# Optimization experiments

Measured on AMD Instinct MI355X. Metric: run time of the kernel, lower is better.

## Reference

```python
import jax, jax.numpy as jnp
import numpy as np
import math

B, S, D, H, KV, HD = 2, 2048, 2048, 32, 8, 64
N_REP = H // KV


def setup_inputs() -> dict:
    key = jax.random.key(0)
    ks = jax.random.split(key, 6)
    x = jax.random.normal(ks[0], (B, S, D), jnp.float32)
    # torch Linear weights, stored as [in, out] for x @ w
    wq = jax.random.normal(ks[1], (D, H * HD), jnp.float32) * 0.02
    wk = jax.random.normal(ks[2], (D, KV * HD), jnp.float32) * 0.02
    wv = jax.random.normal(ks[3], (D, KV * HD), jnp.float32) * 0.02
    wo = jax.random.normal(ks[4], (H * HD, D), jnp.float32) * 0.02
    # rotary angle table: theta[t, j] = t / 10000^(2j/head_dim)
    inv_freq = 1.0 / (10000.0 ** (jnp.arange(0, HD, 2, dtype=jnp.float32) / HD))
    freqs = jnp.arange(S, dtype=jnp.float32)[:, None] * inv_freq[None, :]  # [S, HD//2]
    mask = jnp.triu(jnp.full((S, S), -1e9, dtype=jnp.float32), k=1)
    return {"x": x, "wq": wq, "wk": wk, "wv": wv, "wo": wo,
            "freqs": freqs, "mask": mask, "start_pos": 0}


def _apply_rope(t, cos, sin):
    # t: [b, s, h, d]; pairs are adjacent (llama complex convention)
    b, s, h, d = t.shape
    t2 = t.reshape(b, s, h, d // 2, 2)
    tr, ti = t2[..., 0], t2[..., 1]
    c = cos[None, :, None, :]
    sn = sin[None, :, None, :]
    out_r = tr * c - ti * sn
    out_i = tr * sn + ti * c
    return jnp.stack([out_r, out_i], axis=-1).reshape(b, s, h, d)


def reference(x, wq, wk, wv, wo, freqs, mask, start_pos):
    bsz, seqlen, _ = x.shape
    cos, sin = jnp.cos(freqs), jnp.sin(freqs)
    xq = (x @ wq).reshape(bsz, seqlen, H, HD)
    xk = (x @ wk).reshape(bsz, seqlen, KV, HD)
    xv = (x @ wv).reshape(bsz, seqlen, KV, HD)
    xq = _apply_rope(xq, cos, sin)
    xk = _apply_rope(xk, cos, sin)
    # start_pos == 0 prefill: cache slice [:start_pos+seqlen] == fresh k/v
    keys = jnp.repeat(xk, N_REP, axis=2)    # [b, s, H, hd]
    values = jnp.repeat(xv, N_REP, axis=2)
    q = xq.transpose(0, 2, 1, 3)            # [b, H, s, hd]
    k = keys.transpose(0, 2, 1, 3)
    v = values.transpose(0, 2, 1, 3)
    scores = jnp.einsum('bhqd,bhkd->bhqk', q, k) / math.sqrt(HD)
    scores = scores + mask[None, None, :, :]
    probs = jax.nn.softmax(scores.astype(jnp.float32), axis=-1).astype(q.dtype)
    out = jnp.einsum('bhqk,bhkd->bhqd', probs, v)
    out = out.transpose(0, 2, 1, 3).reshape(bsz, seqlen, H * HD)
    return out @ wo
```

## Files before the change

kernel.cpp:

```cpp
#include <hip/hip_runtime.h>

typedef __attribute__((ext_vector_type(8))) __bf16 bf16x8;
typedef __attribute__((ext_vector_type(4)))  float f32x4;
typedef __attribute__((ext_vector_type(16))) float f32x16;

__device__ __forceinline__ unsigned short f2bfu(float x) {
  union { float f; unsigned u; } v; v.f = x;
  unsigned r = v.u + 0x7fffu + ((v.u >> 16) & 1u);
  return (unsigned short)(r >> 16);
}
__device__ __forceinline__ float bf2f(unsigned short u) {
  union { unsigned u; float f; } v; v.u = ((unsigned)u) << 16;
  return v.f;
}
__device__ __forceinline__ unsigned pkbf(float a, float b) {
  return (unsigned)f2bfu(a) | ((unsigned)f2bfu(b) << 16);
}
__device__ __forceinline__ unsigned pk2(float a, float b) {
  union { __bf16 h[2]; unsigned u; } t;
  t.h[0] = (__bf16)a; t.h[1] = (__bf16)b;
  return t.u;
}
__device__ __forceinline__ void gload16(const void* g, void* l) {
  __builtin_amdgcn_global_load_lds((const __attribute__((address_space(1))) unsigned*)g,
                                   (__attribute__((address_space(3))) unsigned*)l, 16, 0, 0);
}
__device__ __forceinline__ bf16x8 mk8(unsigned a, unsigned b, unsigned c, unsigned d) {
  union { unsigned u[4]; bf16x8 v; } t;
  t.u[0] = a; t.u[1] = b; t.u[2] = c; t.u[3] = d; return t.v;
}

__global__ void cvt_kernel(const float* __restrict__ s, short* __restrict__ d, int n) {
  int i = (blockIdx.x * 256 + threadIdx.x) * 4;
  if (i >= n) return;
  float4 v = *(const float4*)(s + i);
  short4 o;
  o.x = (short)f2bfu(v.x); o.y = (short)f2bfu(v.y);
  o.z = (short)f2bfu(v.z); o.w = (short)f2bfu(v.w);
  *(short4*)(d + i) = o;
}

__global__ void transcvt_kernel(const float* __restrict__ src, short* __restrict__ dst,
                                int R, int C) {
  __shared__ __align__(16) float tl[64][65];
  int c0 = blockIdx.x * 64, r0 = blockIdx.y * 64;
  int t = threadIdx.x;
  int tr = t >> 4, tc = (t & 15) * 4;
#pragma unroll
  for (int i = 0; i < 4; i++) {
    int r = i * 16 + tr;
    float4 v = *(const float4*)(src + (size_t)(r0 + r) * C + c0 + tc);
    tl[r][tc] = v.x; tl[r][tc + 1] = v.y; tl[r][tc + 2] = v.z; tl[r][tc + 3] = v.w;
  }
  __syncthreads();
#pragma unroll
  for (int i = 0; i < 4; i++) {
    int cr = i * 16 + tr;
    short4 o;
    o.x = (short)f2bfu(tl[tc][cr]);
    o.y = (short)f2bfu(tl[tc + 1][cr]);
    o.z = (short)f2bfu(tl[tc + 2][cr]);
    o.w = (short)f2bfu(tl[tc + 3][cr]);
    *(short4*)(dst + (size_t)(c0 + cr) * R + r0 + tc) = o;
  }
}

__global__ void sincos_kernel(const float* __restrict__ freqs, float* __restrict__ ct,
                              float* __restrict__ st) {
  int i = blockIdx.x * 256 + threadIdx.x;
  float f = freqs[i];
  ct[i] = cosf(f);
  st[i] = sinf(f);
}

template <int OUTF32>
__global__ __launch_bounds__(256) void gemm_bt(const short* __restrict__ A,
                                               const short* __restrict__ Bt,
                                               void* __restrict__ C, int M, int N, int K) {
  __shared__ __align__(16) short Al[128 * 32];
  __shared__ __align__(16) short Bl[128 * 32];
  const int t = threadIdx.x, lane = t & 63, w = t >> 6;
  const int m0 = blockIdx.x * 128, n0 = blockIdx.y * 128;
  const int wm = (w & 1) * 64, wn = (w >> 1) * 64;
  f32x4 acc[4][4];
#pragma unroll
  for (int i = 0; i < 4; i++)
#pragma unroll
    for (int j = 0; j < 4; j++)
#pragma unroll
      for (int r = 0; r < 4; r++) acc[i][j][r] = 0.f;

  const int sr = t >> 2;
  const int ss = t & 3;
  const int ldsbase = w * 512;

  for (int k0 = 0; k0 < K; k0 += 32) {
    __syncthreads();
#pragma unroll
    for (int p = 0; p < 2; p++) {
      int r = p * 64 + sr;
      int c = 8 * (ss ^ ((r >> 1) & 3));
      gload16(A + (size_t)(m0 + r) * K + k0 + c, &Al[p * 2048 + ldsbase]);
      gload16(Bt + (size_t)(n0 + r) * K + k0 + c, &Bl[p * 2048 + ldsbase]);
    }
    __syncthreads();
    bf16x8 af[4], bg[4];
#pragma unroll
    for (int i = 0; i < 4; i++) {
      int ra = wm + i * 16 + (lane & 15);
      int sa = (lane >> 4) ^ ((ra >> 1) & 3);
      af[i] = *(const bf16x8*)(&Al[ra * 32 + sa * 8]);
      int rb = wn + i * 16 + (lane & 15);
      int sb = (lane >> 4) ^ ((rb >> 1) & 3);
      bg[i] = *(const bf16x8*)(&Bl[rb * 32 + sb * 8]);
    }
#pragma unroll
    for (int i = 0; i < 4; i++)
#pragma unroll
      for (int j = 0; j < 4; j++)
        acc[i][j] = __builtin_amdgcn_mfma_f32_16x16x32_bf16(af[i], bg[j], acc[i][j], 0, 0, 0);
  }
  const int cr = (lane >> 4) * 4, cc = lane & 15;
#pragma unroll
  for (int i = 0; i < 4; i++)
#pragma unroll
    for (int j = 0; j < 4; j++)
#pragma unroll
      for (int r = 0; r < 4; r++) {
        size_t idx = (size_t)(m0 + wm + i * 16 + cr + r) * N + (n0 + wn + j * 16 + cc);
        if (OUTF32) ((float*)C)[idx] = acc[i][j][r];
        else        ((short*)C)[idx] = (short)f2bfu(acc[i][j][r]);
      }
}

__global__ void rope_kernel(short* __restrict__ qkv, const float* __restrict__ ct,
                            const float* __restrict__ st) {
  int idx = blockIdx.x * 256 + threadIdx.x;
  const int PQ = 4096 * 1024;
  int row, col, i;
  if (idx < PQ) {
    row = idx >> 10; int p = idx & 1023; int h = p >> 5; i = p & 31;
    col = h * 64 + 2 * i;
  } else {
    int k = idx - PQ; row = k >> 8; int p = k & 255; int kvh = p >> 5; i = p & 31;
    col = 2048 + kvh * 64 + 2 * i;
  }
  int s = row & 2047;
  unsigned* ptr = (unsigned*)(qkv + (size_t)row * 3072 + col);
  unsigned v = *ptr;
  float tr = bf2f((unsigned short)(v & 0xffff));
  float ti = bf2f((unsigned short)(v >> 16));
  float c = ct[(s << 5) + i], sn = st[(s << 5) + i];
  *ptr = pkbf(tr * c - ti * sn, tr * sn + ti * c);
}

__global__ void transv_kernel(const short* __restrict__ qkv, short* __restrict__ vt) {
  __shared__ __align__(16) short tl[64][72];
  int st0 = blockIdx.x * 64;
  int bkv = blockIdx.y; int b = bkv >> 3, kv = bkv & 7;
  int t = threadIdx.x;
  int rr = t >> 3, c8 = (t & 7) * 8;
#pragma unroll
  for (int i = 0; i < 2; i++) {
    int sl = i * 32 + rr;
    bf16x8 v = *(const bf16x8*)(qkv + (size_t)(b * 2048 + st0 + sl) * 3072 + 2560 + kv * 64 + c8);
    union { bf16x8 v; short s[8]; } u; u.v = v;
#pragma unroll
    for (int j = 0; j < 8; j++) tl[sl][c8 + j] = u.s[j];
  }
  __syncthreads();
#pragma unroll
  for (int i = 0; i < 2; i++) {
    int dl = i * 32 + rr;
    union { bf16x8 v; short s[8]; } o;
#pragma unroll
    for (int j = 0; j < 8; j++) o.s[j] = tl[c8 + j][dl];
    *(bf16x8*)(vt + ((size_t)(bkv * 64 + dl)) * 2048 + st0 + c8) = o.v;
  }
}

__global__ __launch_bounds__(256) void attn_kernel(const short* __restrict__ qkv,
                                                   const short* __restrict__ vt,
                                                   short* __restrict__ attn) {
  const int S = 2048, NC = 3072;
  __shared__ __align__(16) short sh[2][2][64 * 64];

  const int y = blockIdx.y;
  const int qi = (y < 8) ? y : (23 - y);
  const int qb = qi * 128;
  const int h = blockIdx.x, b = blockIdx.z;
  const int kvh = h >> 2;
  const int t = threadIdx.x, lane = t & 63, w = t >> 6;
  const int q0 = qb + w * 32;
  const int qc = lane & 31, hi = lane >> 5;
  const int qg = q0 + qc;

  bf16x8 bq[4];
  {
    const short* qp = qkv + (size_t)(b * S + qg) * NC + h * 64 + hi * 8;
    const float SC = 0.18033688011112042f;
#pragma unroll
    for (int kk = 0; kk < 4; kk++) {
      union { bf16x8 v; unsigned short s[8]; } u, o;
      u.v = *(const bf16x8*)(qp + kk * 16);
#pragma unroll
      for (int j = 0; j < 8; j++) o.s[j] = f2bfu(bf2f(u.s[j]) * SC);
      bq[kk] = o.v;
    }
  }

  f32x16 ot0, ot1;
#pragma unroll
  for (int r = 0; r < 16; r++) { ot0[r] = 0.f; ot1[r] = 0.f; }
  float m = -1e30f, l = 0.f;

  const int r8 = lane >> 3, sl8 = lane & 7;
  const int scol0 = 8 * (sl8 ^ ((r8 + w) & 7));
  const int scol1 = 8 * (sl8 ^ ((r8 + 4 + w) & 7));
  const short* kptr = qkv + (size_t)(b * S + w * 8 + r8) * NC + 2048 + kvh * 64;
  const short* vptr = vt + (size_t)((b * 8 + kvh) * 64 + w * 8 + r8) * S;

  const int nt = (qb >> 6) + 2;

#define STAGE(tt, bb)                                                                   \
  do {                                                                                  \
    gload16(kptr + (size_t)((tt) * 64) * NC + scol0,        &sh[bb][0][(w * 8) * 64]);  \
    gload16(kptr + (size_t)((tt) * 64 + 32) * NC + scol1,   &sh[bb][0][(32 + w * 8) * 64]); \
    gload16(vptr + (size_t)(tt) * 64 + scol0,               &sh[bb][1][(w * 8) * 64]);  \
    gload16(vptr + (size_t)32 * S + (tt) * 64 + scol1,      &sh[bb][1][(32 + w * 8) * 64]); \
  } while (0)

  STAGE(0, 0);
  __syncthreads();

  for (int tt = 0; tt < nt; ++tt) {
    const int cur = tt & 1;
    if (tt + 1 < nt) STAGE(tt + 1, cur ^ 1);
    const int s0 = tt * 64;
    const short* kb = &sh[cur][0][0];
    const short* vb = &sh[cur][1][0];

    f32x16 cs0, cs1;
#pragma unroll
    for (int r = 0; r < 16; r++) { cs0[r] = 0.f; cs1[r] = 0.f; }
    const int kr0 = lane & 31, kr1 = kr0 + 32;
    const int sw0 = (kr0 + (kr0 >> 3)) & 7, sw1 = (kr1 + (kr1 >> 3)) & 7;
#pragma unroll
    for (int kk = 0; kk < 4; kk++) {
      bf16x8 a0 = *(const bf16x8*)(kb + kr0 * 64 + ((2 * kk + hi) ^ sw0) * 8);
      cs0 = __builtin_amdgcn_mfma_f32_32x32x16_bf16(a0, bq[kk], cs0, 0, 0, 0);
      bf16x8 a1 = *(const bf16x8*)(kb + kr1 * 64 + ((2 * kk + hi) ^ sw1) * 8);
      cs1 = __builtin_amdgcn_mfma_f32_32x32x16_bf16(a1, bq[kk], cs1, 0, 0, 0);
    }

    if (s0 + 63 > q0) {
      const int qrel = qg - s0;
#pragma unroll
      for (int r = 0; r < 16; r++) {
        const int k0 = (r & 3) + 8 * (r >> 2) + 4 * hi;
        if (k0 > qrel)      cs0[r] = -1e30f;
        if (k0 + 32 > qrel) cs1[r] = -1e30f;
      }
    }

    float mx = fmaxf(cs0[0], cs1[0]);
#pragma unroll
    for (int r = 1; r < 16; r++) mx = fmaxf(mx, fmaxf(cs0[r], cs1[r]));
    mx = fmaxf(mx, __shfl_xor(mx, 32, 64));
    if (!__all(mx - m <= 8.f)) {
      const float mn = fmaxf(m, mx);
      const float rf = exp2f(m - mn);
      m = mn;
      l *= rf;
#pragma unroll
      for (int r = 0; r < 16; r++) { ot0[r] *= rf; ot1[r] *= rf; }
    }
    float ls = 0.f;
#pragma unroll
    for (int r = 0; r < 16; r++) { cs0[r] = exp2f(cs0[r] - m); ls += cs0[r]; }
#pragma unroll
    for (int r = 0; r < 16; r++) { cs1[r] = exp2f(cs1[r] - m); ls += cs1[r]; }
    l += ls;

    unsigned x0[8], y0[8], x1[8], y1[8];
#pragma unroll
    for (int j = 0; j < 8; j++) x0[j] = pk2(cs0[2 * j], cs0[2 * j + 1]);
#pragma unroll
    for (int j = 0; j < 8; j++) y0[j] = (unsigned)__shfl_xor((int)x0[j], 32, 64);
#pragma unroll
    for (int j = 0; j < 8; j++) x1[j] = pk2(cs1[2 * j], cs1[2 * j + 1]);
#pragma unroll
    for (int j = 0; j < 8; j++) y1[j] = (unsigned)__shfl_xor((int)x1[j], 32, 64);
    bf16x8 pb0 = hi ? mk8(y0[2], y0[3], x0[2], x0[3]) : mk8(x0[0], x0[1], y0[0], y0[1]);
    bf16x8 pb1 = hi ? mk8(y0[6], y0[7], x0[6], x0[7]) : mk8(x0[4], x0[5], y0[4], y0[5]);
    bf16x8 pb2 = hi ? mk8(y1[2], y1[3], x1[2], x1[3]) : mk8(x1[0], x1[1], y1[0], y1[1]);
    bf16x8 pb3 = hi ? mk8(y1[6], y1[7], x1[6], x1[7]) : mk8(x1[4], x1[5], y1[4], y1[5]);

    const int dl = lane & 31;
    {
      const int d = dl;
      const int swd = (d + (d >> 3)) & 7;
      bf16x8 v0 = *(const bf16x8*)(vb + d * 64 + ((0 + hi) ^ swd) * 8);
      bf16x8 v1 = *(const bf16x8*)(vb + d * 64 + ((2 + hi) ^ swd) * 8);
      bf16x8 v2 = *(const bf16x8*)(vb + d * 64 + ((4 + hi) ^ swd) * 8);
      bf16x8 v3 = *(const bf16x8*)(vb + d * 64 + ((6 + hi) ^ swd) * 8);
      ot0 = __builtin_amdgcn_mfma_f32_32x32x16_bf16(v0, pb0, ot0, 0, 0, 0);
      ot0 = __builtin_amdgcn_mfma_f32_32x32x16_bf16(v1, pb1, ot0, 0, 0, 0);
      ot0 = __builtin_amdgcn_mfma_f32_32x32x16_bf16(v2, pb2, ot0, 0, 0, 0);
      ot0 = __builtin_amdgcn_mfma_f32_32x32x16_bf16(v3, pb3, ot0, 0, 0, 0);
    }
    {
      const int d = 32 + dl;
      const int swd = (d + (d >> 3)) & 7;
      bf16x8 v0 = *(const bf16x8*)(vb + d * 64 + ((0 + hi) ^ swd) * 8);
      bf16x8 v1 = *(const bf16x8*)(vb + d * 64 + ((2 + hi) ^ swd) * 8);
      bf16x8 v2 = *(const bf16x8*)(vb + d * 64 + ((4 + hi) ^ swd) * 8);
      bf16x8 v3 = *(const bf16x8*)(vb + d * 64 + ((6 + hi) ^ swd) * 8);
      ot1 = __builtin_amdgcn_mfma_f32_32x32x16_bf16(v0, pb0, ot1, 0, 0, 0);
      ot1 = __builtin_amdgcn_mfma_f32_32x32x16_bf16(v1, pb1, ot1, 0, 0, 0);
      ot1 = __builtin_amdgcn_mfma_f32_32x32x16_bf16(v2, pb2, ot1, 0, 0, 0);
      ot1 = __builtin_amdgcn_mfma_f32_32x32x16_bf16(v3, pb3, ot1, 0, 0, 0);
    }
    __syncthreads();
  }
#undef STAGE

  short (*ol)[32 * 72] = (short (*)[32 * 72]) & sh[0][0][0];
  float lt = l + __shfl_xor(l, 32, 64);
  float inv = 1.0f / lt;
#pragma unroll
  for (int dh = 0; dh < 2; dh++) {
#pragma unroll
    for (int j = 0; j < 8; j++) {
      int d = ((2 * j) & 3) + 8 * ((2 * j) >> 2) + 4 * hi + 32 * dh;
      float a = (dh ? ot1[2 * j] : ot0[2 * j]) * inv;
      float bb = (dh ? ot1[2 * j + 1] : ot0[2 * j + 1]) * inv;
      *(unsigned*)(&ol[w][qc * 72 + d]) = pkbf(a, bb);
    }
  }
  __syncthreads();
  const int qr = lane >> 1, part = lane & 1;
  short* og = attn + (size_t)(b * S + q0 + qr) * 2048 + h * 64 + part * 32;
  const short* ip = &ol[w][qr * 72 + part * 32];
#pragma unroll
  for (int i2 = 0; i2 < 4; i2++) *(bf16x8*)(og + i2 * 8) = *(const bf16x8*)(ip + i2 * 8);
}

extern "C" void kernel_launch(void* const* d_in, const int* in_sizes, int n_in,
                              void* d_out, int out_size, void* d_ws, size_t ws_size,
                              hipStream_t stream) {
  (void)in_sizes; (void)n_in; (void)out_size; (void)ws_size;
  const float* x     = (const float*)d_in[0];
  const float* wq    = (const float*)d_in[1];
  const float* wk    = (const float*)d_in[2];
  const float* wv    = (const float*)d_in[3];
  const float* wo    = (const float*)d_in[4];
  const float* freqs = (const float*)d_in[5];

  char* ws = (char*)d_ws;
  short* qkv  = (short*)(ws + 0);
  short* vtb  = (short*)(ws + 25165824);
  short* xb   = (short*)(ws + 29360128);
  short* attn = xb;
  short* wT   = (short*)(ws + 46137344);
  float* ct   = (float*)(ws + 58720256);
  float* st   = (float*)(ws + 58982400);

  cvt_kernel<<<8192, 256, 0, stream>>>(x, xb, 8388608);
  transcvt_kernel<<<dim3(32, 32), 256, 0, stream>>>(wq, wT, 2048, 2048);
  transcvt_kernel<<<dim3(8, 32), 256, 0, stream>>>(wk, wT + (size_t)2048 * 2048, 2048, 512);
  transcvt_kernel<<<dim3(8, 32), 256, 0, stream>>>(wv, wT + (size_t)2560 * 2048, 2048, 512);
  sincos_kernel<<<256, 256, 0, stream>>>(freqs, ct, st);
  gemm_bt<0><<<dim3(32, 24), 256, 0, stream>>>(xb, wT, qkv, 4096, 3072, 2048);
  transcvt_kernel<<<dim3(32, 32), 256, 0, stream>>>(wo, wT, 2048, 2048);
  rope_kernel<<<20480, 256, 0, stream>>>(qkv, ct, st);
  transv_kernel<<<dim3(32, 16), 256, 0, stream>>>(qkv, vtb);
  attn_kernel<<<dim3(32, 16, 2), 256, 0, stream>>>(qkv, vtb, attn);
  gemm_bt<1><<<dim3(32, 16), 256, 0, stream>>>(attn, wT, d_out, 4096, 2048, 2048);
}
```

Before: 383.5 us.

## Replace GEMM with double-buffered 256x256 tile kernel and XCD-aware block swizzle

The QKV and output-projection GEMMs move from 128x128 tiles with 256 threads to 256x256 tiles with 512 threads. The new kernel double-buffers the LDS loads so global-to-LDS copies overlap the MFMA work, and it remaps block IDs across the 8 XCDs. This is meant to raise data reuse per tile and hide load latency. The attention kernel also gets s_setprio around its MFMA sections. Larger tiles mean fewer blocks: 192 and 128 of them, which may underfill 256 CUs, and higher register use per thread.

Result: slower. 392.3 us (+2.3%).

```diff
diff --git a/kernel.cpp b/kernel.cpp
--- a/kernel.cpp
+++ b/kernel.cpp
@@ -74,60 +74,75 @@
 }
 
 template <int OUTF32>
-__global__ __launch_bounds__(256) void gemm_bt(const short* __restrict__ A,
-                                               const short* __restrict__ Bt,
-                                               void* __restrict__ C, int M, int N, int K) {
-  __shared__ __align__(16) short Al[128 * 32];
-  __shared__ __align__(16) short Bl[128 * 32];
+__global__ __launch_bounds__(512, 2) void gemm256(const short* __restrict__ A,
+                                                  const short* __restrict__ Bt,
+                                                  void* __restrict__ C, int N, int K) {
+  __shared__ __align__(16) short lds[2][2][256 * 32];
   const int t = threadIdx.x, lane = t & 63, w = t >> 6;
-  const int m0 = blockIdx.x * 128, n0 = blockIdx.y * 128;
-  const int wm = (w & 1) * 64, wn = (w >> 1) * 64;
-  f32x4 acc[4][4];
-#pragma unroll
-  for (int i = 0; i < 4; i++)
+  const int nwg = gridDim.x * gridDim.y;
+  int bid = blockIdx.x + gridDim.x * blockIdx.y;
+  const int qq = nwg >> 3;
+  bid = (bid & 7) * qq + (bid >> 3);
+  const int m0 = (bid % gridDim.x) * 256;
+  const int n0 = (bid / gridDim.x) * 256;
+  const int wm = w & 1, wn = w >> 1;
+
+  f32x4 acc[8][4];
+#pragma unroll
+  for (int i = 0; i < 8; i++)
 #pragma unroll
     for (int j = 0; j < 4; j++)
 #pragma unroll
       for (int r = 0; r < 4; r++) acc[i][j][r] = 0.f;
 
-  const int sr = t >> 2;
-  const int ss = t & 3;
-  const int ldsbase = w * 512;
-
-  for (int k0 = 0; k0 < K; k0 += 32) {
+  const int srow = w * 16 + (lane >> 2);
+  const int scol = 8 * ((lane & 3) ^ ((lane >> 3) & 3));
+  const short* Ap = A + (size_t)(m0 + srow) * K + scol;
+  const short* Bp = Bt + (size_t)(n0 + srow) * K + scol;
+  const int ldsw = (w * 16) * 32;
+
+#define SG(k0, bb)                                                        \
+  do {                                                                    \
+    gload16(Ap + (size_t)(k0),                 &lds[bb][0][ldsw]);        \
+    gload16(Ap + (size_t)128 * K + (k0),       &lds[bb][0][4096 + ldsw]); \
+    gload16(Bp + (size_t)(k0),                 &lds[bb][1][ldsw]);        \
+    gload16(Bp + (size_t)128 * K + (k0),       &lds[bb][1][4096 + ldsw]); \
+  } while (0)
+
+  SG(0, 0);
+  __syncthreads();
+
+  const int fr = lane & 15, fs = lane >> 4;
+  const int p8 = (fs ^ ((fr >> 1) & 3)) * 8;
+  const int nt = K >> 5;
+  for (int tl = 0; tl < nt; ++tl) {
+    const int cur = tl & 1;
+    if (tl + 1 < nt) SG((size_t)(tl + 1) * 32, cur ^ 1);
+    const short* ba = &lds[cur][0][0];
+    const short* bb_ = &lds[cur][1][0];
+    bf16x8 bg[4];
+#pragma unroll
+    for (int j = 0; j < 4; j++)
+      bg[j] = *(const bf16x8*)(bb_ + (wn * 64 + j * 16 + fr) * 32 + p8);
+#pragma unroll
+    for (int i = 0; i < 8; i++) {
+      bf16x8 af = *(const bf16x8*)(ba + (wm * 128 + i * 16 + fr) * 32 + p8);
+#pragma unroll
+      for (int j = 0; j < 4; j++)
+        acc[i][j] = __builtin_amdgcn_mfma_f32_16x16x32_bf16(af, bg[j], acc[i][j], 0, 0, 0);
+    }
     __syncthreads();
-#pragma unroll
-    for (int p = 0; p < 2; p++) {
-      int r = p * 64 + sr;
-      int c = 8 * (ss ^ ((r >> 1) & 3));
-      gload16(A + (size_t)(m0 + r) * K + k0 + c, &Al[p * 2048 + ldsbase]);
-      gload16(Bt + (size_t)(n0 + r) * K + k0 + c, &Bl[p * 2048 + ldsbase]);
-    }
-    __syncthreads();
-    bf16x8 af[4], bg[4];
-#pragma unroll
-    for (int i = 0; i < 4; i++) {
-      int ra = wm + i * 16 + (lane & 15);
-      int sa = (lane >> 4) ^ ((ra >> 1) & 3);
-      af[i] = *(const bf16x8*)(&Al[ra * 32 + sa * 8]);
-      int rb = wn + i * 16 + (lane & 15);
-      int sb = (lane >> 4) ^ ((rb >> 1) & 3);
-      bg[i] = *(const bf16x8*)(&Bl[rb * 32 + sb * 8]);
-    }
-#pragma unroll
-    for (int i = 0; i < 4; i++)
-#pragma unroll
-      for (int j = 0; j < 4; j++)
-        acc[i][j] = __builtin_amdgcn_mfma_f32_16x16x32_bf16(af[i], bg[j], acc[i][j], 0, 0, 0);
-  }
-  const int cr = (lane >> 4) * 4, cc = lane & 15;
-#pragma unroll
-  for (int i = 0; i < 4; i++)
+  }
+#undef SG
+
+  const int cr = fs * 4, cc = fr;
+#pragma unroll
+  for (int i = 0; i < 8; i++)
 #pragma unroll
     for (int j = 0; j < 4; j++)
 #pragma unroll
       for (int r = 0; r < 4; r++) {
-        size_t idx = (size_t)(m0 + wm + i * 16 + cr + r) * N + (n0 + wn + j * 16 + cc);
+        size_t idx = (size_t)(m0 + wm * 128 + i * 16 + cr + r) * N + (n0 + wn * 64 + j * 16 + cc);
         if (OUTF32) ((float*)C)[idx] = acc[i][j][r];
         else        ((short*)C)[idx] = (short)f2bfu(acc[i][j][r]);
       }
@@ -245,6 +260,7 @@
     for (int r = 0; r < 16; r++) { cs0[r] = 0.f; cs1[r] = 0.f; }
     const int kr0 = lane & 31, kr1 = kr0 + 32;
     const int sw0 = (kr0 + (kr0 >> 3)) & 7, sw1 = (kr1 + (kr1 >> 3)) & 7;
+    __builtin_amdgcn_s_setprio(1);
 #pragma unroll
     for (int kk = 0; kk < 4; kk++) {
       bf16x8 a0 = *(const bf16x8*)(kb + kr0 * 64 + ((2 * kk + hi) ^ sw0) * 8);
@@ -252,6 +268,7 @@
       bf16x8 a1 = *(const bf16x8*)(kb + kr1 * 64 + ((2 * kk + hi) ^ sw1) * 8);
       cs1 = __builtin_amdgcn_mfma_f32_32x32x16_bf16(a1, bq[kk], cs1, 0, 0, 0);
     }
+    __builtin_amdgcn_s_setprio(0);
 
     if (s0 + 63 > q0) {
       const int qrel = qg - s0;
@@ -297,6 +314,7 @@
     bf16x8 pb3 = hi ? mk8(y1[6], y1[7], x1[6], x1[7]) : mk8(x1[4], x1[5], y1[4], y1[5]);
 
     const int dl = lane & 31;
+    __builtin_amdgcn_s_setprio(1);
     {
       const int d = dl;
       const int swd = (d + (d >> 3)) & 7;
@@ -321,6 +339,7 @@
       ot1 = __builtin_amdgcn_mfma_f32_32x32x16_bf16(v2, pb2, ot1, 0, 0, 0);
       ot1 = __builtin_amdgcn_mfma_f32_32x32x16_bf16(v3, pb3, ot1, 0, 0, 0);
     }
+    __builtin_amdgcn_s_setprio(0);
     __syncthreads();
   }
 #undef STAGE
@@ -371,10 +390,10 @@
   transcvt_kernel<<<dim3(8, 32), 256, 0, stream>>>(wk, wT + (size_t)2048 * 2048, 2048, 512);
   transcvt_kernel<<<dim3(8, 32), 256, 0, stream>>>(wv, wT + (size_t)2560 * 2048, 2048, 512);
   sincos_kernel<<<256, 256, 0, stream>>>(freqs, ct, st);
-  gemm_bt<0><<<dim3(32, 24), 256, 0, stream>>>(xb, wT, qkv, 4096, 3072, 2048);
+  gemm256<0><<<dim3(16, 12), 512, 0, stream>>>(xb, wT, qkv, 3072, 2048);
   transcvt_kernel<<<dim3(32, 32), 256, 0, stream>>>(wo, wT, 2048, 2048);
   rope_kernel<<<20480, 256, 0, stream>>>(qkv, ct, st);
   transv_kernel<<<dim3(32, 16), 256, 0, stream>>>(qkv, vtb);
   attn_kernel<<<dim3(32, 16, 2), 256, 0, stream>>>(qkv, vtb, attn);
-  gemm_bt<1><<<dim3(32, 16), 256, 0, stream>>>(attn, wT, d_out, 4096, 2048, 2048);
-}
+  gemm256<1><<<dim3(16, 8), 512, 0, stream>>>(attn, wT, d_out, 2048, 2048);
+}
```
